# Kernel tuning notes

Hardware: AMD Instinct MI355X
Metric: run time of the kernel (lower is better)

## Reference

```python
import jax, jax.numpy as jnp
import numpy as np

N, D_IN = 8192, 1024
FC1, FC2, FC3 = 256, 128, 64
DQK = FC3 // 8  # 8


def setup_inputs() -> dict:
    key = jax.random.key(0)
    ks = jax.random.split(key, 20)
    s = 0.05
    inp = {
        "x": jax.random.normal(ks[0], (N, D_IN), jnp.float32),
        # feature extractor MLP (dropout omitted: eval mode)
        "W1": jax.random.normal(ks[1], (D_IN, FC1), jnp.float32) * s,
        "b1": jnp.zeros((FC1,), jnp.float32),
        "W2": jax.random.normal(ks[2], (FC1, FC2), jnp.float32) * s,
        "b2": jnp.zeros((FC2,), jnp.float32),
        "W3": jax.random.normal(ks[3], (FC2, FC3), jnp.float32) * s,
        "b3": jnp.zeros((FC3,), jnp.float32),
        # 1x1 conv Q/K/V == linear layers on the 64-dim embedding
        "Wq": jax.random.normal(ks[4], (FC3, DQK), jnp.float32) * s,
        "bq": jnp.zeros((DQK,), jnp.float32),
        "Wk": jax.random.normal(ks[5], (FC3, DQK), jnp.float32) * s,
        "bk": jnp.zeros((DQK,), jnp.float32),
        "Wv": jax.random.normal(ks[6], (FC3, FC3), jnp.float32) * s,
        "bv": jnp.zeros((FC3,), jnp.float32),
        "gamma": jnp.array([0.5], jnp.float32),  # learned residual scale (init 0 in torch)
        # attention-pooling branch
        "Wa1": jax.random.normal(ks[7], (FC3, FC3), jnp.float32) * s,
        "ba1": jnp.zeros((FC3,), jnp.float32),
        "Wa2": jax.random.normal(ks[8], (FC3, 1), jnp.float32) * s,
        "ba2": jnp.zeros((1,), jnp.float32),
        # classifier
        "Wc": jax.random.normal(ks[9], (FC3, 1), jnp.float32) * s,
        "bc": jnp.zeros((1,), jnp.float32),
    }
    return inp


def reference(x, W1, b1, W2, b2, W3, b3, Wq, bq, Wk, bk, Wv, bv, gamma,
              Wa1, ba1, Wa2, ba2, Wc, bc):
    # instance feature extractor (dropout identity at eval)
    H = jax.nn.relu(x @ W1 + b1)
    H = jax.nn.relu(H @ W2 + b2)
    H = jax.nn.relu(H @ W3 + b3)                 # [N, 64]
    # self-attention over instances (unscaled dot product)
    Q = H @ Wq + bq                              # [N, 8]
    K = H @ Wk + bk                              # [N, 8]
    V = H @ Wv + bv                              # [N, 64]
    att = jax.nn.softmax(Q @ K.T, axis=-1)       # [N, N] full score matrix
    H = gamma[0] * (att @ V) + H                 # residual scale-add
    # attention-based MIL pooling
    scores = jnp.tanh(H @ Wa1 + ba1) @ Wa2 + ba2 # [N, 1]
    A = jax.nn.softmax(scores[:, 0])             # [N]
    M = A @ H                                    # [64] bag embedding
    Y = jax.nn.sigmoid(M @ Wc + bc)[0]
    Y_prob = jnp.clip(Y, 1e-5, 1.0 - 1e-5)
    return (Y_prob, M)
```

## Files before the change

kernel.cpp:

```cpp
#include <hip/hip_runtime.h>
#include <math.h>

typedef unsigned short ushort_t;
typedef __attribute__((ext_vector_type(8))) short short8;
typedef __attribute__((ext_vector_type(4))) float f32x4;

__device__ inline unsigned bfpair(float lo, float hi) {
  unsigned r;
  asm("v_cvt_pk_bf16_f32 %0, %1, %2" : "=v"(r) : "v"(lo), "v"(hi));
  return r;
}
__device__ inline ushort_t bf16of(float v) { return (ushort_t)(bfpair(v, v) & 0xffffu); }
__device__ inline void permswap32(unsigned &a, unsigned &b) {
  asm("v_permlane32_swap_b32 %0, %1" : "+v"(a), "+v"(b));
}
__device__ inline void permswap16(unsigned &a, unsigned &b) {
  asm("v_permlane16_swap_b32 %0, %1" : "+v"(a), "+v"(b));
}

__device__ void transpose_tile(const float* __restrict__ W, ushort_t* __restrict__ Wt,
                               int K, int N, int bx, int by, int t)
{
  __shared__ float Ls[32][33];
  const int n0 = bx * 32, k0 = by * 32;
  const int tx = t & 31, tyb = t >> 5;
  #pragma unroll
  for (int s = 0; s < 4; ++s) {
    const int k = tyb + s * 8;
    Ls[k][tx] = W[(size_t)(k0 + k) * N + n0 + tx];
  }
  __syncthreads();
  #pragma unroll
  for (int s = 0; s < 2; ++s) {
    const int idx = t + 256 * s;
    const int n = idx >> 4, kk = (idx & 15) * 2;
    const unsigned pk = bfpair(Ls[kk][n], Ls[kk + 1][n]);
    *(unsigned*)&Wt[(size_t)(n0 + n) * K + k0 + kk] = pk;
  }
}

__global__ __launch_bounds__(256) void prep_all_k(
    const float* __restrict__ W1, ushort_t* __restrict__ W1t,
    const float* __restrict__ W2, ushort_t* __restrict__ W2t,
    const float* __restrict__ W3, ushort_t* __restrict__ W3t,
    const float* __restrict__ Wa1, ushort_t* __restrict__ Wa1t,
    const float* __restrict__ Wq, const float* __restrict__ Wk,
    const float* __restrict__ Wv, ushort_t* __restrict__ WqkvT)
{
  const int bid = blockIdx.x;
  const int t = threadIdx.x;
  if (bid < 256)      { transpose_tile(W1, W1t, 1024, 256, bid & 7, bid >> 3, t); }
  else if (bid < 288) { const int l = bid - 256; transpose_tile(W2, W2t, 256, 128, l & 3, l >> 2, t); }
  else if (bid < 296) { const int l = bid - 288; transpose_tile(W3, W3t, 128,  64, l & 1, l >> 1, t); }
  else if (bid < 300) { const int l = bid - 296; transpose_tile(Wa1, Wa1t, 64,  64, l & 1, l >> 1, t); }
  else {
    for (int e = t; e < 80 * 64; e += 256) {
      const int j = e >> 6, k = e & 63;
      float v;
      if (j < 8)       v = Wq[k * 8 + j];
      else if (j < 16) v = Wk[k * 8 + (j - 8)];
      else             v = Wv[k * 64 + (j - 16)];
      WqkvT[e] = bf16of(v);
    }
  }
}

template<int K, int N, int WAVES, bool A_FP32, int OMODE>
__global__ __launch_bounds__(WAVES * 64) void gemm_staged(
    const void* __restrict__ Ap, const ushort_t* __restrict__ Wt,
    const float* __restrict__ bias, void* __restrict__ C0, void* __restrict__ C1)
{
  constexpr int BM = 32;
  constexpr int NWN = N / 32;
  constexpr int NK = K / 32;
  constexpr int A_CH = BM * 4;
  constexpr int B_CH = N * 4;
  static_assert(WAVES * 64 == B_CH, "threads must equal B chunk count");
  static_assert(A_CH <= WAVES * 64, "");

  const int tid = threadIdx.x;
  const int wave = tid >> 6, lane = tid & 63;
  const int ln = lane & 15, g = lane >> 4;
  const int wm = wave / NWN, wn = wave % NWN;
  const int bm0 = blockIdx.x * BM;

  __shared__ ushort_t Als[2][BM][40];
  __shared__ ushort_t Bls[2][N][40];

  const float* Af = (const float*)Ap;
  const ushort_t* Ab = (const ushort_t*)Ap;

  const bool hasA = (tid < A_CH);
  const int arow = tid >> 2, akq = tid & 3;
  const int bc = hasA ? (B_CH - A_CH + tid) : (tid - A_CH);
  const int brow = bc >> 2, bkq = bc & 3;

  float4 rf0, rf1;
  short8 ra, rb;

  auto LOADK = [&](int ks) {
    const int k0 = ks * 32;
    if (hasA) {
      if (A_FP32) {
        const float* src = &Af[(size_t)(bm0 + arow) * K + k0 + akq * 8];
        rf0 = *(const float4*)src;
        rf1 = *(const float4*)(src + 4);
      } else {
        ra = *(const short8*)&Ab[(size_t)(bm0 + arow) * K + k0 + akq * 8];
      }
    }
    rb = *(const short8*)&Wt[(size_t)brow * K + k0 + bkq * 8];
  };
  auto WRITEK = [&](int cur) {
    if (hasA) {
      short8 wa;
      if (A_FP32) {
        union { unsigned u[4]; short8 s8; } cv;
        cv.u[0] = bfpair(rf0.x, rf0.y);
        cv.u[1] = bfpair(rf0.z, rf0.w);
        cv.u[2] = bfpair(rf1.x, rf1.y);
        cv.u[3] = bfpair(rf1.z, rf1.w);
        wa = cv.s8;
      } else {
        wa = ra;
      }
      *(short8*)&Als[cur][arow][akq * 8] = wa;
    }
    *(short8*)&Bls[cur][brow][bkq * 8] = rb;
  };

  f32x4 acc0 = {0.f, 0.f, 0.f, 0.f};
  f32x4 acc1 = {0.f, 0.f, 0.f, 0.f};

  LOADK(0);
  int cur = 0;
  for (int ks = 0; ks < NK; ++ks) {
    WRITEK(cur);
    __syncthreads();
    if (ks + 1 < NK) LOADK(ks + 1);
    const short8 af = *(const short8*)&Als[cur][wm * 16 + ln][g * 8];
    const short8 b0 = *(const short8*)&Bls[cur][wn * 32 + ln][g * 8];
    const short8 b1 = *(const short8*)&Bls[cur][wn * 32 + 16 + ln][g * 8];
    acc0 = __builtin_amdgcn_mfma_f32_16x16x32_bf16(af, b0, acc0, 0, 0, 0);
    acc1 = __builtin_amdgcn_mfma_f32_16x16x32_bf16(af, b1, acc1, 0, 0, 0);
    cur ^= 1;
  }

  #pragma unroll
  for (int nt = 0; nt < 2; ++nt) {
    const f32x4 a = nt ? acc1 : acc0;
    #pragma unroll
    for (int r = 0; r < 4; ++r) {
      const int m = bm0 + wm * 16 + 4 * g + r;
      const int n = wn * 32 + nt * 16 + ln;
      float v = a[r] + bias[n];
      v = fmaxf(v, 0.f);
      if (OMODE == 0) {
        ((ushort_t*)C0)[(size_t)m * N + n] = bf16of(v);
      } else {
        ((float*)C0)[(size_t)m * N + n] = v;
      }
    }
  }
}

__global__ __launch_bounds__(256) void gemm3_qkv_k(
    const ushort_t* __restrict__ H2b, const ushort_t* __restrict__ W3t,
    const float* __restrict__ b3, const ushort_t* __restrict__ WqkvT,
    const float* __restrict__ bq, const float* __restrict__ bk, const float* __restrict__ bv,
    float* __restrict__ H3, ushort_t* __restrict__ Qb, ushort_t* __restrict__ Kb,
    ushort_t* __restrict__ VT)
{
  const int wave = threadIdx.x >> 6, lane = threadIdx.x & 63;
  const int ln = lane & 15, g = lane >> 4;
  const int q0 = blockIdx.x * 16;
  const f32x4 zero4 = {0.f, 0.f, 0.f, 0.f};

  __shared__ ushort_t Hls[16][72];

  f32x4 acc = zero4;
  #pragma unroll
  for (int k0 = 0; k0 < 128; k0 += 32) {
    const short8 af = *(const short8*)&H2b[(size_t)(q0 + ln) * 128 + k0 + g * 8];
    const short8 bfr = *(const short8*)&W3t[(size_t)(wave * 16 + ln) * 128 + k0 + g * 8];
    acc = __builtin_amdgcn_mfma_f32_16x16x32_bf16(af, bfr, acc, 0, 0, 0);
  }
  #pragma unroll
  for (int r = 0; r < 4; ++r) {
    const int m = q0 + 4 * g + r;
    const int n = wave * 16 + ln;
    float v = fmaxf(acc[r] + b3[n], 0.f);
    H3[(size_t)m * 64 + n] = v;
    Hls[4 * g + r][n] = bf16of(v);
  }
  __syncthreads();

  const int ntA = (wave == 0) ? 0 : (wave + 1);
  f32x4 accA = zero4, accB = zero4;
  #pragma unroll
  for (int k0 = 0; k0 < 64; k0 += 32) {
    const short8 af = *(const short8*)&Hls[ln][k0 + g * 8];
    const short8 bA = *(const short8*)&WqkvT[(size_t)(ntA * 16 + ln) * 64 + k0 + g * 8];
    accA = __builtin_amdgcn_mfma_f32_16x16x32_bf16(af, bA, accA, 0, 0, 0);
    if (wave == 0) {
      const short8 bB = *(const short8*)&WqkvT[(size_t)(16 + ln) * 64 + k0 + g * 8];
      accB = __builtin_amdgcn_mfma_f32_16x16x32_bf16(af, bB, accB, 0, 0, 0);
    }
  }
  if (wave == 0) {
    const float b0 = (ln < 8) ? bq[ln] : bk[ln - 8];
    #pragma unroll
    for (int r = 0; r < 4; ++r) {
      const int m = q0 + 4 * g + r;
      const float v = accA[r] + b0;
      if (ln < 8) Qb[(size_t)m * 8 + ln] = bf16of(v);
      else        Kb[(size_t)m * 8 + (ln - 8)] = bf16of(v);
    }
    const int d = ln;
    const float bb = bv[d];
    uint2 o;
    o.x = bfpair(accB[0] + bb, accB[1] + bb);
    o.y = bfpair(accB[2] + bb, accB[3] + bb);
    *(uint2*)&VT[(size_t)d * 8192 + q0 + 4 * g] = o;
  } else {
    const int d = (ntA - 1) * 16 + ln;
    const float bb = bv[d];
    uint2 o;
    o.x = bfpair(accA[0] + bb, accA[1] + bb);
    o.y = bfpair(accA[2] + bb, accA[3] + bb);
    *(uint2*)&VT[(size_t)d * 8192 + q0 + 4 * g] = o;
  }
}

__global__ __launch_bounds__(1024) void attn_part_k(
    const ushort_t* __restrict__ Qb, const ushort_t* __restrict__ Kb,
    const ushort_t* __restrict__ VT, float* __restrict__ Pnum,
    float* __restrict__ Pden)
{
  const int tid = threadIdx.x;
  const int wave = tid >> 6, lane = tid & 63;
  const int m = lane & 15, g = lane >> 4;
  const int qg = blockIdx.x >> 3, js = blockIdx.x & 7;
  const int q0 = qg * 256 + wave * 16;
  const int j0 = js * 1024;
  const f32x4 zero4 = {0.f,0.f,0.f,0.f};

  __shared__ ushort_t Vls[2][64][68];
  __shared__ ushort_t Kls[2][64][12];

  const bool isV = (tid < 512);
  const int vd = tid >> 3, vc = tid & 7;
  const bool isK = (tid >= 512 && tid < 576);
  const int kj = tid - 512;

  short8 vreg = {0,0,0,0,0,0,0,0}, kreg = {0,0,0,0,0,0,0,0};
  auto LOAD = [&](int jb) {
    if (isV) vreg = *(const short8*)&VT[(size_t)vd * 8192 + jb + vc * 8];
    if (isK) kreg = *(const short8*)&Kb[(size_t)(jb + kj) * 8];
  };
  auto WRITE = [&](int cur) {
    if (isV) *(short8*)&Vls[cur][vd][vc * 8] = vreg;
    if (isK) *(short8*)&Kls[cur][kj][0] = kreg;
  };

  short8 qf = {0,0,0,0,0,0,0,0};
  if (lane < 16) qf = *(const short8*)&Qb[(size_t)(q0 + m) * 8];

  f32x4 acc[4];
  #pragma unroll
  for (int dt=0;dt<4;dt++) acc[dt] = zero4;
  float lsum = 0.f;

  LOAD(j0);
  int cur = 0;
  for (int it = 0; it < 16; ++it) {
    WRITE(cur);
    __syncthreads();
    if (it + 1 < 16) LOAD(j0 + (it + 1) * 64);

    #pragma unroll
    for (int half = 0; half < 2; ++half) {
      short8 kf0 = {0,0,0,0,0,0,0,0}, kf1 = {0,0,0,0,0,0,0,0};
      if (lane < 16) {
        kf0 = *(const short8*)&Kls[cur][half*32 + m][0];
        kf1 = *(const short8*)&Kls[cur][half*32 + 16 + m][0];
      }
      const f32x4 s0 = __builtin_amdgcn_mfma_f32_16x16x32_bf16(kf0, qf, zero4, 0,0,0);
      const f32x4 s1 = __builtin_amdgcn_mfma_f32_16x16x32_bf16(kf1, qf, zero4, 0,0,0);
      const float e00 = __expf(s0[0]), e01 = __expf(s0[1]), e02 = __expf(s0[2]), e03 = __expf(s0[3]);
      const float e10 = __expf(s1[0]), e11 = __expf(s1[1]), e12 = __expf(s1[2]), e13 = __expf(s1[3]);
      lsum += ((e00+e01)+(e02+e03)) + ((e10+e11)+(e12+e13));
      unsigned X01 = bfpair(e00,e01), X23 = bfpair(e02,e03);
      unsigned Y01 = bfpair(e10,e11), Y23 = bfpair(e12,e13);
      permswap32(X01, Y01); permswap16(X01, Y01);
      permswap32(X23, Y23); permswap16(X23, Y23);
      union { unsigned u[4]; short8 s; } pfu;
      pfu.u[0] = X01;
      pfu.u[1] = X23;
      pfu.u[2] = Y01;
      pfu.u[3] = Y23;
      #pragma unroll
      for (int dt=0;dt<4;dt++) {
        const short8 vf = *(const short8*)&Vls[cur][dt*16 + m][half*32 + g * 8];
        acc[dt] = __builtin_amdgcn_mfma_f32_16x16x32_bf16(pfu.s, vf, acc[dt], 0,0,0);
      }
    }
    cur ^= 1;
  }

  lsum += __shfl_xor(lsum, 16, 64);
  lsum += __shfl_xor(lsum, 32, 64);

  float* np = &Pnum[((size_t)blockIdx.x * 256 + wave * 16) * 64];
  #pragma unroll
  for (int dt=0;dt<4;dt++)
    #pragma unroll
    for (int r=0;r<4;r++)
      np[(size_t)(4*g + r) * 64 + dt*16 + m] = acc[dt][r];
  if (lane < 16)
    Pden[(size_t)blockIdx.x * 256 + wave * 16 + m] = lsum;
}

__global__ __launch_bounds__(256) void attn_merge_k(
    const float* __restrict__ Pnum, const float* __restrict__ Pden,
    const float* __restrict__ H3, const float* __restrict__ gamma,
    float* __restrict__ Hatt, ushort_t* __restrict__ Hab)
{
  const int wave = threadIdx.x >> 6, lane = threadIdx.x & 63;
  const int q = blockIdx.x * 4 + wave;
  const int qg = q >> 8, qloc = q & 255;
  float num = 0.f, den = 0.f;
  #pragma unroll
  for (int js = 0; js < 8; ++js) {
    const size_t base = (size_t)(qg * 8 + js) * 256 + qloc;
    num += Pnum[base * 64 + lane];
    den += Pden[base];
  }
  const float hv = fmaf(gamma[0], num / den, H3[(size_t)q * 64 + lane]);
  Hatt[(size_t)q * 64 + lane] = hv;
  Hab[(size_t)q * 64 + lane] = bf16of(hv);
}

__global__ __launch_bounds__(64) void mil_fused_k(
    const ushort_t* __restrict__ Hab, const ushort_t* __restrict__ Wa1t,
    const float* __restrict__ ba1, const float* __restrict__ Wa2,
    const float* __restrict__ ba2, float* __restrict__ scores)
{
  const int lane = threadIdx.x;
  const int ln = lane & 15, g = lane >> 4;
  const int q0 = blockIdx.x * 16;
  const f32x4 zero4 = {0.f, 0.f, 0.f, 0.f};
  f32x4 acc[4];
  #pragma unroll
  for (int nt = 0; nt < 4; ++nt) acc[nt] = zero4;
  #pragma unroll
  for (int k0 = 0; k0 < 64; k0 += 32) {
    const short8 af = *(const short8*)&Hab[(size_t)(q0 + ln) * 64 + k0 + g * 8];
    #pragma unroll
    for (int nt = 0; nt < 4; ++nt) {
      const short8 bfr = *(const short8*)&Wa1t[(size_t)(nt * 16 + ln) * 64 + k0 + g * 8];
      acc[nt] = __builtin_amdgcn_mfma_f32_16x16x32_bf16(af, bfr, acc[nt], 0, 0, 0);
    }
  }
  #pragma unroll
  for (int r = 0; r < 4; ++r) {
    float s = 0.f;
    #pragma unroll
    for (int nt = 0; nt < 4; ++nt) {
      const int n = nt * 16 + ln;
      s += tanhf(acc[nt][r] + ba1[n]) * Wa2[n];
    }
    s += __shfl_xor(s, 1, 64); s += __shfl_xor(s, 2, 64);
    s += __shfl_xor(s, 4, 64); s += __shfl_xor(s, 8, 64);
    if (ln == 0) scores[q0 + 4 * g + r] = s + ba2[0];
  }
}

__global__ __launch_bounds__(256) void pool1_k(
    const float* __restrict__ Hm, const float* __restrict__ scores,
    float* __restrict__ pM, float* __restrict__ pS)
{
  const int wave = threadIdx.x >> 6, lane = threadIdx.x & 63;
  const int b = blockIdx.x;
  float macc = 0.f, se = 0.f;
  for (int t=0;t<32;t++) {
    const int i = b*128 + wave*32 + t;
    const float e = __expf(scores[i]);
    se += e;
    macc = fmaf(e, Hm[(size_t)i*64 + lane], macc);
  }
  __shared__ float Ms[4][64];
  __shared__ float Ss[4];
  Ms[wave][lane] = macc;
  if (lane == 0) Ss[wave] = se;
  __syncthreads();
  if (wave == 0) {
    pM[b*64 + lane] = Ms[0][lane]+Ms[1][lane]+Ms[2][lane]+Ms[3][lane];
    if (lane == 0) pS[b] = Ss[0]+Ss[1]+Ss[2]+Ss[3];
  }
}

__global__ void pool2_k(const float* __restrict__ pM, const float* __restrict__ pS,
                        const float* __restrict__ Wc, const float* __restrict__ bc,
                        float* __restrict__ out)
{
  const int lane = threadIdx.x;
  float s_ = pS[lane];
  s_ += __shfl_xor(s_,1,64);  s_ += __shfl_xor(s_,2,64);
  s_ += __shfl_xor(s_,4,64);  s_ += __shfl_xor(s_,8,64);
  s_ += __shfl_xor(s_,16,64); s_ += __shfl_xor(s_,32,64);
  float m_ = 0.f;
  for (int b=0;b<64;b++) m_ += pM[b*64+lane];
  const float Md = m_ / s_;
  out[1+lane] = Md;
  float yp = Md * Wc[lane];
  yp += __shfl_xor(yp,1,64);  yp += __shfl_xor(yp,2,64);
  yp += __shfl_xor(yp,4,64);  yp += __shfl_xor(yp,8,64);
  yp += __shfl_xor(yp,16,64); yp += __shfl_xor(yp,32,64);
  if (lane == 0) {
    float y = 1.f/(1.f + __expf(-(yp + bc[0])));
    y = fminf(fmaxf(y, 1e-5f), 1.f - 1e-5f);
    out[0] = y;
  }
}

extern "C" void kernel_launch(void* const* d_in, const int* in_sizes, int n_in,
                              void* d_out, int out_size, void* d_ws, size_t ws_size,
                              hipStream_t stream)
{
  const float* x    = (const float*)d_in[0];
  const float* W1   = (const float*)d_in[1];
  const float* b1   = (const float*)d_in[2];
  const float* W2   = (const float*)d_in[3];
  const float* b2   = (const float*)d_in[4];
  const float* W3   = (const float*)d_in[5];
  const float* b3   = (const float*)d_in[6];
  const float* Wq   = (const float*)d_in[7];
  const float* bq   = (const float*)d_in[8];
  const float* Wk   = (const float*)d_in[9];
  const float* bk   = (const float*)d_in[10];
  const float* Wv   = (const float*)d_in[11];
  const float* bv   = (const float*)d_in[12];
  const float* gam  = (const float*)d_in[13];
  const float* Wa1  = (const float*)d_in[14];
  const float* ba1  = (const float*)d_in[15];
  const float* Wa2  = (const float*)d_in[16];
  const float* ba2  = (const float*)d_in[17];
  const float* Wc   = (const float*)d_in[18];
  const float* bc   = (const float*)d_in[19];
  float* out = (float*)d_out;

  char* w = (char*)d_ws;
  float* H3 = (float*)w;        w += (size_t)8192*64*4;
  float* Ha = (float*)w;        w += (size_t)8192*64*4;
  float* sc = (float*)w;        w += 8192*4;
  float* pM = (float*)w;        w += 64*64*4;
  float* pS = (float*)w;        w += 64*4;
  float* Pnum = (float*)w;      w += (size_t)256*256*64*4;
  float* Pden = (float*)w;      w += (size_t)256*256*4;
  ushort_t* H1b = (ushort_t*)w; w += (size_t)8192*256*2;
  ushort_t* H2b = (ushort_t*)w; w += (size_t)8192*128*2;
  ushort_t* Hab = (ushort_t*)w; w += (size_t)8192*64*2;
  ushort_t* Qb  = (ushort_t*)w; w += (size_t)8192*8*2;
  ushort_t* Kb  = (ushort_t*)w; w += (size_t)8192*8*2;
  ushort_t* VT  = (ushort_t*)w; w += (size_t)64*8192*2;
  ushort_t* W1t = (ushort_t*)w; w += (size_t)256*1024*2;
  ushort_t* W2t = (ushort_t*)w; w += (size_t)128*256*2;
  ushort_t* W3t = (ushort_t*)w; w += (size_t)64*128*2;
  ushort_t* Wa1t= (ushort_t*)w; w += (size_t)64*64*2;
  ushort_t* Wqkv= (ushort_t*)w; w += (size_t)80*64*2;

  prep_all_k<<<301, 256, 0, stream>>>(W1, W1t, W2, W2t, W3, W3t, Wa1, Wa1t,
                                      Wq, Wk, Wv, Wqkv);

  gemm_staged<1024,256,16,true ,0><<<256, 1024, 0, stream>>>(x,   W1t, b1, H1b, nullptr);
  gemm_staged< 256,128, 8,false,0><<<256,  512, 0, stream>>>(H1b, W2t, b2, H2b, nullptr);
  gemm3_qkv_k<<<512, 256, 0, stream>>>(H2b, W3t, b3, Wqkv, bq, bk, bv, H3, Qb, Kb, VT);

  attn_part_k<<<256, 1024, 0, stream>>>(Qb, Kb, VT, Pnum, Pden);
  attn_merge_k<<<2048, 256, 0, stream>>>(Pnum, Pden, H3, gam, Ha, Hab);
  mil_fused_k<<<512, 64, 0, stream>>>(Hab, Wa1t, ba1, Wa2, ba2, sc);
  pool1_k<<<64, 256, 0, stream>>>(Ha, sc, pM, pS);
  pool2_k<<<1, 64, 0, stream>>>(pM, pS, Wc, bc, out);
}
```

Measured before the change: 82.32 us.

## Fuse MLP layers 2-3 with QKV and merge attention epilogue kernels

Folds the second MLP GEMM into the layer-3/QKV kernel, so H2 is kept in shared memory rather than written to and re-read from global memory. It also merges the attention merge, the MIL scoring GEMM and the first pooling stage into one epilogue kernel that holds H and its bf16 copy in LDS, removing the Ha, Hab and scores round trips and three launches. The trade-off is less parallelism: the epilogue runs on only 128 blocks instead of 2048, and layer 2 now recomputes per 16-row tile with W2 loaded from global memory by each block.

```diff
diff --git a/kernel.cpp b/kernel.cpp
--- a/kernel.cpp
+++ b/kernel.cpp
@@ -164,8 +164,9 @@
   }
 }
 
-__global__ __launch_bounds__(256) void gemm3_qkv_k(
-    const ushort_t* __restrict__ H2b, const ushort_t* __restrict__ W3t,
+__global__ __launch_bounds__(256) void mlp23_qkv_k(
+    const ushort_t* __restrict__ H1b, const ushort_t* __restrict__ W2t,
+    const float* __restrict__ b2, const ushort_t* __restrict__ W3t,
     const float* __restrict__ b3, const ushort_t* __restrict__ WqkvT,
     const float* __restrict__ bq, const float* __restrict__ bk, const float* __restrict__ bv,
     float* __restrict__ H3, ushort_t* __restrict__ Qb, ushort_t* __restrict__ Kb,
@@ -176,20 +177,39 @@
   const int q0 = blockIdx.x * 16;
   const f32x4 zero4 = {0.f, 0.f, 0.f, 0.f};
 
+  __shared__ ushort_t H2ls[16][136];
   __shared__ ushort_t Hls[16][72];
 
-  f32x4 acc = zero4;
+  f32x4 a2[2] = {zero4, zero4};
+  #pragma unroll 2
+  for (int k0 = 0; k0 < 256; k0 += 32) {
+    const short8 af = *(const short8*)&H1b[(size_t)(q0 + ln) * 256 + k0 + g * 8];
+    const short8 b0 = *(const short8*)&W2t[(size_t)(wave * 32 + ln) * 256 + k0 + g * 8];
+    const short8 b1 = *(const short8*)&W2t[(size_t)(wave * 32 + 16 + ln) * 256 + k0 + g * 8];
+    a2[0] = __builtin_amdgcn_mfma_f32_16x16x32_bf16(af, b0, a2[0], 0, 0, 0);
+    a2[1] = __builtin_amdgcn_mfma_f32_16x16x32_bf16(af, b1, a2[1], 0, 0, 0);
+  }
+  #pragma unroll
+  for (int nt = 0; nt < 2; ++nt)
+    #pragma unroll
+    for (int r = 0; r < 4; ++r) {
+      const int n = wave * 32 + nt * 16 + ln;
+      H2ls[4 * g + r][n] = bf16of(fmaxf(a2[nt][r] + b2[n], 0.f));
+    }
+  __syncthreads();
+
+  f32x4 a3 = zero4;
   #pragma unroll
   for (int k0 = 0; k0 < 128; k0 += 32) {
-    const short8 af = *(const short8*)&H2b[(size_t)(q0 + ln) * 128 + k0 + g * 8];
+    const short8 af = *(const short8*)&H2ls[ln][k0 + g * 8];
     const short8 bfr = *(const short8*)&W3t[(size_t)(wave * 16 + ln) * 128 + k0 + g * 8];
-    acc = __builtin_amdgcn_mfma_f32_16x16x32_bf16(af, bfr, acc, 0, 0, 0);
+    a3 = __builtin_amdgcn_mfma_f32_16x16x32_bf16(af, bfr, a3, 0, 0, 0);
   }
   #pragma unroll
   for (int r = 0; r < 4; ++r) {
     const int m = q0 + 4 * g + r;
     const int n = wave * 16 + ln;
-    float v = fmaxf(acc[r] + b3[n], 0.f);
+    float v = fmaxf(a3[r] + b3[n], 0.f);
     H3[(size_t)m * 64 + n] = v;
     Hls[4 * g + r][n] = bf16of(v);
   }
@@ -321,41 +341,47 @@
     Pden[(size_t)blockIdx.x * 256 + wave * 16 + m] = lsum;
 }
 
-__global__ __launch_bounds__(256) void attn_merge_k(
+__global__ __launch_bounds__(256) void epilogue_k(
     const float* __restrict__ Pnum, const float* __restrict__ Pden,
     const float* __restrict__ H3, const float* __restrict__ gamma,
-    float* __restrict__ Hatt, ushort_t* __restrict__ Hab)
+    const ushort_t* __restrict__ Wa1t, const float* __restrict__ ba1,
+    const float* __restrict__ Wa2, const float* __restrict__ ba2,
+    float* __restrict__ pM, float* __restrict__ pS)
 {
   const int wave = threadIdx.x >> 6, lane = threadIdx.x & 63;
-  const int q = blockIdx.x * 4 + wave;
-  const int qg = q >> 8, qloc = q & 255;
-  float num = 0.f, den = 0.f;
-  #pragma unroll
-  for (int js = 0; js < 8; ++js) {
-    const size_t base = (size_t)(qg * 8 + js) * 256 + qloc;
-    num += Pnum[base * 64 + lane];
-    den += Pden[base];
-  }
-  const float hv = fmaf(gamma[0], num / den, H3[(size_t)q * 64 + lane]);
-  Hatt[(size_t)q * 64 + lane] = hv;
-  Hab[(size_t)q * 64 + lane] = bf16of(hv);
-}
-
-__global__ __launch_bounds__(64) void mil_fused_k(
-    const ushort_t* __restrict__ Hab, const ushort_t* __restrict__ Wa1t,
-    const float* __restrict__ ba1, const float* __restrict__ Wa2,
-    const float* __restrict__ ba2, float* __restrict__ scores)
-{
-  const int lane = threadIdx.x;
   const int ln = lane & 15, g = lane >> 4;
-  const int q0 = blockIdx.x * 16;
+  const int q0 = blockIdx.x * 64 + wave * 16;
   const f32x4 zero4 = {0.f, 0.f, 0.f, 0.f};
+
+  __shared__ float Hals[4][16][68];
+  __shared__ ushort_t Habls[4][16][72];
+  __shared__ float scls[4][16];
+  __shared__ float Ms[4][64];
+  __shared__ float Ss[4];
+
+  const float gm = gamma[0];
+  #pragma unroll 4
+  for (int r = 0; r < 16; ++r) {
+    const int q = q0 + r;
+    const int qg = q >> 8, qloc = q & 255;
+    float num = 0.f, den = 0.f;
+    #pragma unroll
+    for (int js = 0; js < 8; ++js) {
+      const size_t base = (size_t)(qg * 8 + js) * 256 + qloc;
+      num += Pnum[base * 64 + lane];
+      den += Pden[base];
+    }
+    const float hv = fmaf(gm, num / den, H3[(size_t)q * 64 + lane]);
+    Hals[wave][r][lane] = hv;
+    Habls[wave][r][lane] = bf16of(hv);
+  }
+
   f32x4 acc[4];
   #pragma unroll
   for (int nt = 0; nt < 4; ++nt) acc[nt] = zero4;
   #pragma unroll
   for (int k0 = 0; k0 < 64; k0 += 32) {
-    const short8 af = *(const short8*)&Hab[(size_t)(q0 + ln) * 64 + k0 + g * 8];
+    const short8 af = *(const short8*)&Habls[wave][ln][k0 + g * 8];
     #pragma unroll
     for (int nt = 0; nt < 4; ++nt) {
       const short8 bfr = *(const short8*)&Wa1t[(size_t)(nt * 16 + ln) * 64 + k0 + g * 8];
@@ -372,31 +398,22 @@
     }
     s += __shfl_xor(s, 1, 64); s += __shfl_xor(s, 2, 64);
     s += __shfl_xor(s, 4, 64); s += __shfl_xor(s, 8, 64);
-    if (ln == 0) scores[q0 + 4 * g + r] = s + ba2[0];
-  }
-}
-
-__global__ __launch_bounds__(256) void pool1_k(
-    const float* __restrict__ Hm, const float* __restrict__ scores,
-    float* __restrict__ pM, float* __restrict__ pS)
-{
-  const int wave = threadIdx.x >> 6, lane = threadIdx.x & 63;
-  const int b = blockIdx.x;
+    if (ln == 0) scls[wave][4 * g + r] = s + ba2[0];
+  }
+
   float macc = 0.f, se = 0.f;
-  for (int t=0;t<32;t++) {
-    const int i = b*128 + wave*32 + t;
-    const float e = __expf(scores[i]);
+  #pragma unroll 4
+  for (int r = 0; r < 16; ++r) {
+    const float e = __expf(scls[wave][r]);
     se += e;
-    macc = fmaf(e, Hm[(size_t)i*64 + lane], macc);
-  }
-  __shared__ float Ms[4][64];
-  __shared__ float Ss[4];
+    macc = fmaf(e, Hals[wave][r][lane], macc);
+  }
   Ms[wave][lane] = macc;
   if (lane == 0) Ss[wave] = se;
   __syncthreads();
   if (wave == 0) {
-    pM[b*64 + lane] = Ms[0][lane]+Ms[1][lane]+Ms[2][lane]+Ms[3][lane];
-    if (lane == 0) pS[b] = Ss[0]+Ss[1]+Ss[2]+Ss[3];
+    pM[(size_t)blockIdx.x * 64 + lane] = Ms[0][lane] + Ms[1][lane] + Ms[2][lane] + Ms[3][lane];
+    if (lane == 0) pS[blockIdx.x] = Ss[0] + Ss[1] + Ss[2] + Ss[3];
   }
 }
 
@@ -405,14 +422,14 @@
                         float* __restrict__ out)
 {
   const int lane = threadIdx.x;
-  float s_ = pS[lane];
+  float s_ = pS[lane] + pS[64 + lane];
   s_ += __shfl_xor(s_,1,64);  s_ += __shfl_xor(s_,2,64);
   s_ += __shfl_xor(s_,4,64);  s_ += __shfl_xor(s_,8,64);
   s_ += __shfl_xor(s_,16,64); s_ += __shfl_xor(s_,32,64);
   float m_ = 0.f;
-  for (int b=0;b<64;b++) m_ += pM[b*64+lane];
+  for (int b = 0; b < 128; ++b) m_ += pM[b * 64 + lane];
   const float Md = m_ / s_;
-  out[1+lane] = Md;
+  out[1 + lane] = Md;
   float yp = Md * Wc[lane];
   yp += __shfl_xor(yp,1,64);  yp += __shfl_xor(yp,2,64);
   yp += __shfl_xor(yp,4,64);  yp += __shfl_xor(yp,8,64);
@@ -452,15 +469,11 @@
 
   char* w = (char*)d_ws;
   float* H3 = (float*)w;        w += (size_t)8192*64*4;
-  float* Ha = (float*)w;        w += (size_t)8192*64*4;
-  float* sc = (float*)w;        w += 8192*4;
-  float* pM = (float*)w;        w += 64*64*4;
-  float* pS = (float*)w;        w += 64*4;
+  float* pM = (float*)w;        w += 128*64*4;
+  float* pS = (float*)w;        w += 128*4;
   float* Pnum = (float*)w;      w += (size_t)256*256*64*4;
   float* Pden = (float*)w;      w += (size_t)256*256*4;
   ushort_t* H1b = (ushort_t*)w; w += (size_t)8192*256*2;
-  ushort_t* H2b = (ushort_t*)w; w += (size_t)8192*128*2;
-  ushort_t* Hab = (ushort_t*)w; w += (size_t)8192*64*2;
   ushort_t* Qb  = (ushort_t*)w; w += (size_t)8192*8*2;
   ushort_t* Kb  = (ushort_t*)w; w += (size_t)8192*8*2;
   ushort_t* VT  = (ushort_t*)w; w += (size_t)64*8192*2;
@@ -472,14 +485,10 @@
 
   prep_all_k<<<301, 256, 0, stream>>>(W1, W1t, W2, W2t, W3, W3t, Wa1, Wa1t,
                                       Wq, Wk, Wv, Wqkv);
-
-  gemm_staged<1024,256,16,true ,0><<<256, 1024, 0, stream>>>(x,   W1t, b1, H1b, nullptr);
-  gemm_staged< 256,128, 8,false,0><<<256,  512, 0, stream>>>(H1b, W2t, b2, H2b, nullptr);
-  gemm3_qkv_k<<<512, 256, 0, stream>>>(H2b, W3t, b3, Wqkv, bq, bk, bv, H3, Qb, Kb, VT);
-
+  gemm_staged<1024,256,16,true ,0><<<256, 1024, 0, stream>>>(x, W1t, b1, H1b, nullptr);
+  mlp23_qkv_k<<<512, 256, 0, stream>>>(H1b, W2t, b2, W3t, b3, Wqkv,
+                                       bq, bk, bv, H3, Qb, Kb, VT);
   attn_part_k<<<256, 1024, 0, stream>>>(Qb, Kb, VT, Pnum, Pden);
-  attn_merge_k<<<2048, 256, 0, stream>>>(Pnum, Pden, H3, gam, Ha, Hab);
-  mil_fused_k<<<512, 64, 0, stream>>>(Hab, Wa1t, ba1, Wa2, ba2, sc);
-  pool1_k<<<64, 256, 0, stream>>>(Ha, sc, pM, pS);
+  epilogue_k<<<128, 256, 0, stream>>>(Pnum, Pden, H3, gam, Wa1t, ba1, Wa2, ba2, pM, pS);
   pool2_k<<<1, 64, 0, stream>>>(pM, pS, Wc, bc, out);
 }
```

Result: faster. 79.00 us (-4.0%).
